# Kernel tuning notes

Hardware: AMD Instinct MI355X
Metric: run time of the kernel (lower is better)

Reference implementation:

```python
import jax, jax.numpy as jnp
import numpy as np

WIN = 7
SHIFT = 3
HEADS = 4
DIM = 128


def _rel_pos_index(wh, ww):
    coords = np.stack(np.meshgrid(np.arange(wh), np.arange(ww), indexing='ij')).reshape(2, -1)
    rel = (coords[:, :, None] - coords[:, None, :]).transpose(1, 2, 0)  # (N,N,2)
    rel[..., 0] += wh - 1
    rel[..., 1] += ww - 1
    rel[..., 0] *= 2 * ww - 1
    return rel.sum(-1)  # (N,N) int


def _shift_mask(H, W, wh, ww, sh, sw):
    img = np.zeros((H, W), dtype=np.float32)
    cnt = 0
    for hs in (slice(0, -wh), slice(-wh, -sh), slice(-sh, None)):
        for ws in (slice(0, -ww), slice(-ww, -sw), slice(-sw, None)):
            img[hs, ws] = cnt
            cnt += 1
    mw = img.reshape(H // wh, wh, W // ww, ww).transpose(0, 2, 1, 3).reshape(-1, wh * ww)
    diff = mw[:, :, None] - mw[:, None, :]
    return np.where(diff != 0, -100.0, 0.0).astype(np.float32)  # (nW,N,N)


def setup_inputs() -> dict:
    key = jax.random.key(0)
    ks = jax.random.split(key, 5)
    x = jax.random.normal(ks[0], (16, 112, 112, DIM), dtype=jnp.float32)
    w_qkv = jax.random.normal(ks[1], (DIM, 3 * DIM), dtype=jnp.float32) * 0.02
    b_qkv = jnp.zeros((3 * DIM,), dtype=jnp.float32)
    w_proj = jax.random.normal(ks[2], (DIM, DIM), dtype=jnp.float32) * 0.02
    b_proj = jnp.zeros((DIM,), dtype=jnp.float32)
    log_sigma = jnp.zeros((HEADS,), dtype=jnp.float32)  # sigma=1.0
    bias_table = jax.random.normal(ks[3], ((2 * WIN - 1) ** 2, HEADS), dtype=jnp.float32) * 0.02
    return {"x": x, "w_qkv": w_qkv, "b_qkv": b_qkv, "w_proj": w_proj,
            "b_proj": b_proj, "log_sigma": log_sigma, "bias_table": bias_table}


def reference(x, w_qkv, b_qkv, w_proj, b_proj, log_sigma, bias_table):
    B, H, W, C = x.shape
    wh = ww = WIN
    sh = sw = SHIFT
    heads = HEADS
    hd = C // heads
    N = wh * ww
    nWh, nWw = H // wh, W // ww

    shifted = jnp.roll(x, (-sh, -sw), axis=(1, 2))
    qkv = shifted @ w_qkv + b_qkv  # (B,H,W,3C)
    # window partition: -> (B*nW, 3, heads, N, hd)
    qkv = qkv.reshape(B, nWh, wh, nWw, ww, 3, heads, hd)
    qkv = qkv.transpose(0, 1, 3, 5, 6, 2, 4, 7).reshape(B * nWh * nWw, 3, heads, N, hd)
    q, k, v = qkv[:, 0], qkv[:, 1], qkv[:, 2]

    scale = hd ** -0.5
    q = q * scale
    k = k * scale
    q_sq = jnp.sum(q * q, -1, keepdims=True)               # (B_,h,N,1)
    k_sq = jnp.sum(k * k, -1, keepdims=True).swapaxes(-2, -1)  # (B_,h,1,N)
    qk = jnp.einsum('bhnd,bhmd->bhnm', q, k)
    dist_sq = jnp.maximum(q_sq + k_sq - 2.0 * qk, 1e-12)
    sigma_sq = jnp.exp(2.0 * log_sigma).reshape(1, heads, 1, 1)
    attn = (-0.5 / sigma_sq) * dist_sq                     # (B_,h,N,N)

    rpi = jnp.asarray(_rel_pos_index(wh, ww))
    bias = bias_table[rpi.reshape(-1)].reshape(N, N, heads).transpose(2, 0, 1)
    attn = attn + bias[None]

    mask = jnp.asarray(_shift_mask(H, W, wh, ww, sh, sw))  # (nW,N,N)
    attn = attn.reshape(B, nWh * nWw, heads, N, N) + mask[None, :, None]
    attn = jax.nn.softmax(attn, axis=-1).reshape(-1, heads, N, N)

    out = jnp.einsum('bhnm,bhmd->bhnd', attn, v)           # (B_,h,N,hd)
    out = out.transpose(0, 2, 1, 3).reshape(B, nWh, nWw, wh, ww, C)
    out = out.transpose(0, 1, 3, 2, 4, 5).reshape(B, H, W, C)
    out = jnp.roll(out, (sh, sw), axis=(1, 2))
    return out @ w_proj + b_proj
```

## Files before the change

kernel.cpp:

```cpp
#include <hip/hip_runtime.h>
#include <math.h>

#define IMG 112
#define CDIM 128
#define NTOK 49

__global__ __launch_bounds__(256, 4) void qkv_gemm_kernel(
    const float* __restrict__ x, const float* __restrict__ w,
    const float* __restrict__ bqkv, float* __restrict__ qkv)
{
    __shared__ float At[32][132];
    __shared__ float Bs[32][132];
    const int tid = threadIdx.x;
    const int m0 = blockIdx.x << 7;
    const int j0 = blockIdx.y << 7;
    const int tm = tid >> 4, tn = tid & 15;
    const float fscale = (j0 < 256) ? 0.17677669529663687f : 1.0f;

    float acc[8][8];
#pragma unroll
    for (int i = 0; i < 8; i++)
#pragma unroll
        for (int j = 0; j < 8; j++) acc[i][j] = 0.0f;

    for (int kc = 0; kc < 4; kc++) {
        if (kc) __syncthreads();
#pragma unroll
        for (int i = 0; i < 4; i++) {
            int idx = tid + (i << 8);
            int r = idx >> 3;
            int c4 = (idx & 7) << 2;
            int m = m0 + r;
            int b = m / (IMG * IMG);
            int rem = m - b * (IMG * IMG);
            int hh = rem / IMG;
            int ww_ = rem - hh * IMG;
            int hs = hh + 3; if (hs >= IMG) hs -= IMG;
            int ws = ww_ + 3; if (ws >= IMG) ws -= IMG;
            float4 v = *(const float4*)(x + ((size_t)((b * IMG + hs) * IMG + ws)) * CDIM + (kc << 5) + c4);
            At[c4 + 0][r] = v.x;
            At[c4 + 1][r] = v.y;
            At[c4 + 2][r] = v.z;
            At[c4 + 3][r] = v.w;
        }
#pragma unroll
        for (int i = 0; i < 4; i++) {
            int idx = tid + (i << 8);
            int c = idx >> 5;
            int j4 = (idx & 31) << 2;
            *(float4*)(&Bs[c][j4]) = *(const float4*)(w + (size_t)((kc << 5) + c) * 384 + j0 + j4);
        }
        __syncthreads();
#pragma unroll
        for (int c = 0; c < 32; c++) {
            float4 a0 = *(const float4*)(&At[c][tm << 2]);
            float4 a1 = *(const float4*)(&At[c][64 + (tm << 2)]);
            float4 b0 = *(const float4*)(&Bs[c][tn << 2]);
            float4 b1 = *(const float4*)(&Bs[c][64 + (tn << 2)]);
            float av[8] = {a0.x, a0.y, a0.z, a0.w, a1.x, a1.y, a1.z, a1.w};
            float bv[8] = {b0.x, b0.y, b0.z, b0.w, b1.x, b1.y, b1.z, b1.w};
#pragma unroll
            for (int ii = 0; ii < 8; ii++)
#pragma unroll
                for (int jj = 0; jj < 8; jj++) acc[ii][jj] = fmaf(av[ii], bv[jj], acc[ii][jj]);
        }
    }
    const int jb0 = j0 + (tn << 2);
    float4 bq0 = *(const float4*)(bqkv + jb0);
    float4 bq1 = *(const float4*)(bqkv + jb0 + 64);
#pragma unroll
    for (int ih = 0; ih < 2; ih++) {
#pragma unroll
        for (int ii = 0; ii < 4; ii++) {
            int r = (ih << 6) + (tm << 2) + ii;
            int m = m0 + r;
            int b = m / (IMG * IMG);
            int rem = m - b * (IMG * IMG);
            int hh = rem / IMG;
            int ww_ = rem - hh * IMG;
            int wi = hh / 7, ph = hh - wi * 7;
            int wj = ww_ / 7, pw = ww_ - wj * 7;
            size_t mp = (size_t)(((b * 16 + wi) * 16 + wj) * 49 + ph * 7 + pw);
            int ai = (ih << 2) + ii;
            float4 o0, o1;
            o0.x = (acc[ai][0] + bq0.x) * fscale;
            o0.y = (acc[ai][1] + bq0.y) * fscale;
            o0.z = (acc[ai][2] + bq0.z) * fscale;
            o0.w = (acc[ai][3] + bq0.w) * fscale;
            o1.x = (acc[ai][4] + bq1.x) * fscale;
            o1.y = (acc[ai][5] + bq1.y) * fscale;
            o1.z = (acc[ai][6] + bq1.z) * fscale;
            o1.w = (acc[ai][7] + bq1.w) * fscale;
            *(float4*)(qkv + mp * 384 + jb0) = o0;
            *(float4*)(qkv + mp * 384 + jb0 + 64) = o1;
        }
    }
}

#define KVSLAB 3136
#define OFF_BT 12544
#define SM_FLOATS 13220

__global__ __launch_bounds__(256, 3) void attn_kernel(
    const float* __restrict__ qkv, const float* __restrict__ wproj,
    const float* __restrict__ bproj, const float* __restrict__ lsig,
    const float* __restrict__ btab, float* __restrict__ out)
{
    __shared__ float sm[SM_FLOATS];
    const int tid = threadIdx.x;
    const int lane = tid & 63;
    const int h = tid >> 6;
    const int bx = blockIdx.x;
    const int wi = (bx >> 4) & 15;
    const int wj = bx & 15;

    float* kh  = sm + h * KVSLAB;
    float* vh  = kh + 1568;
    float* bts = sm + OFF_BT;
    float* osb = sm;
    float* wp  = sm + 6272;

    for (int i = tid; i < 676; i += 256) bts[i] = btab[i];

    const bool fi = (wi == 15), fj = (wj == 15);
    float4 q[8];
    float qsq = 0.0f, ks = 0.0f;
    int pbit = 0, qbit = 0, rbase = 0;

    const float* blkbase = qkv + (size_t)bx * (49 * 384);

    if (lane < NTOK) {
        int nh_ = lane / 7, nw_ = lane - (lane / 7) * 7;
        rbase = (nh_ * 13 + nw_) * 4 + h;
        pbit = (nh_ < 4) ? 1 : 0;
        qbit = (nw_ < 4) ? 1 : 0;
        const float* rowp = blkbase + lane * 384 + h * 32;
#pragma unroll
        for (int d4 = 0; d4 < 8; d4++) {
            float4 qv = *(const float4*)(rowp + (d4 << 2));
            q[d4] = qv;
            qsq = fmaf(qv.x, qv.x, qsq); qsq = fmaf(qv.y, qv.y, qsq);
            qsq = fmaf(qv.z, qv.z, qsq); qsq = fmaf(qv.w, qv.w, qsq);
            float4 kv = *(const float4*)(rowp + 128 + (d4 << 2));
            ks = fmaf(kv.x, kv.x, ks); ks = fmaf(kv.y, kv.y, ks);
            ks = fmaf(kv.z, kv.z, ks); ks = fmaf(kv.w, kv.w, ks);
            *(float4*)(kh + lane * 32 + ((d4 ^ (lane & 7)) << 2)) = kv;
            float4 vv = *(const float4*)(rowp + 256 + (d4 << 2));
            *(float4*)(vh + lane * 32 + ((d4 ^ (lane & 7)) << 2)) = vv;
        }
    }
    __syncthreads();

    float4 o[8];
#pragma unroll
    for (int d4 = 0; d4 < 8; d4++) { o[d4].x = 0.f; o[d4].y = 0.f; o[d4].z = 0.f; o[d4].w = 0.f; }
    float inv = 0.0f;

    if (lane < NTOK) {
        const float coef = -0.5f * __expf(-2.0f * lsig[h]);
        float s[49];
#pragma unroll
        for (int m = 0; m < 49; m++) {
            const int mh = m / 7, mw = m - (m / 7) * 7;
            float qk = 0.0f;
#pragma unroll
            for (int d4 = 0; d4 < 8; d4++) {
                float4 k4 = *(const float4*)(kh + m * 32 + ((d4 ^ (m & 7)) << 2));
                qk = fmaf(q[d4].x, k4.x, qk); qk = fmaf(q[d4].y, k4.y, qk);
                qk = fmaf(q[d4].z, k4.z, qk); qk = fmaf(q[d4].w, k4.w, qk);
            }
            float ksm = __shfl(ks, m, 64);
            float dist = fmaxf(qsq + ksm - 2.0f * qk, 1e-12f);
            float bias = bts[rbase + ((6 - mh) * 13 + (6 - mw)) * 4];
            int msk = (fi ? (pbit ^ ((mh < 4) ? 1 : 0)) : 0) | (fj ? (qbit ^ ((mw < 4) ? 1 : 0)) : 0);
            s[m] = fmaf(coef, dist, msk ? bias - 100.0f : bias);
        }
        float mx = s[0];
#pragma unroll
        for (int m = 1; m < 49; m++) mx = fmaxf(mx, s[m]);
        float sum = 0.0f;
#pragma unroll
        for (int m = 0; m < 49; m++) { float e = __expf(s[m] - mx); s[m] = e; sum += e; }
        inv = 1.0f / sum;
#pragma unroll
        for (int m = 0; m < 49; m++) {
            const float p = s[m];
#pragma unroll
            for (int d4 = 0; d4 < 8; d4++) {
                float4 v4 = *(const float4*)(vh + m * 32 + ((d4 ^ (m & 7)) << 2));
                o[d4].x = fmaf(p, v4.x, o[d4].x);
                o[d4].y = fmaf(p, v4.y, o[d4].y);
                o[d4].z = fmaf(p, v4.z, o[d4].z);
                o[d4].w = fmaf(p, v4.w, o[d4].w);
            }
        }
    }
    __syncthreads();

    if (lane < NTOK) {
#pragma unroll
        for (int d4 = 0; d4 < 8; d4++) {
            float4 ov;
            ov.x = o[d4].x * inv; ov.y = o[d4].y * inv;
            ov.z = o[d4].z * inv; ov.w = o[d4].w * inv;
            int gg = (h << 3) + d4;
            *(float4*)(osb + lane * 128 + ((gg ^ (lane & 7)) << 2)) = ov;
        }
    }
    for (int i = tid; i < 1024; i += 256)
        ((float4*)wp)[i] = ((const float4*)wproj)[i];
    __syncthreads();

    const int e4 = tid & 31;
    const int rowbase = tid >> 5;
    float4 bv = *(const float4*)(bproj + (e4 << 2));
    float4 pacc[7];
#pragma unroll
    for (int r = 0; r < 7; r++) pacc[r] = bv;

    for (int ch = 0; ch < 4; ch++) {
#pragma unroll 4
        for (int c4 = 0; c4 < 8; c4++) {
            const int cb = c4 << 2;
            float4 w0 = *(const float4*)(wp + (cb + 0) * 128 + (e4 << 2));
            float4 w1 = *(const float4*)(wp + (cb + 1) * 128 + (e4 << 2));
            float4 w2 = *(const float4*)(wp + (cb + 2) * 128 + (e4 << 2));
            float4 w3 = *(const float4*)(wp + (cb + 3) * 128 + (e4 << 2));
            const int gg = (ch << 3) + c4;
#pragma unroll
            for (int r = 0; r < 7; r++) {
                int nn = rowbase + (r << 3);
                if (nn < NTOK) {
                    float4 o4 = *(const float4*)(osb + nn * 128 + ((gg ^ (nn & 7)) << 2));
                    float4 a = pacc[r];
                    a.x = fmaf(o4.x, w0.x, a.x); a.y = fmaf(o4.x, w0.y, a.y);
                    a.z = fmaf(o4.x, w0.z, a.z); a.w = fmaf(o4.x, w0.w, a.w);
                    a.x = fmaf(o4.y, w1.x, a.x); a.y = fmaf(o4.y, w1.y, a.y);
                    a.z = fmaf(o4.y, w1.z, a.z); a.w = fmaf(o4.y, w1.w, a.w);
                    a.x = fmaf(o4.z, w2.x, a.x); a.y = fmaf(o4.z, w2.y, a.y);
                    a.z = fmaf(o4.z, w2.z, a.z); a.w = fmaf(o4.z, w2.w, a.w);
                    a.x = fmaf(o4.w, w3.x, a.x); a.y = fmaf(o4.w, w3.y, a.y);
                    a.z = fmaf(o4.w, w3.z, a.z); a.w = fmaf(o4.w, w3.w, a.w);
                    pacc[r] = a;
                }
            }
        }
        if (ch < 3) {
            __syncthreads();
            for (int i = tid; i < 1024; i += 256)
                ((float4*)wp)[i] = ((const float4*)(wproj + ((ch + 1) << 12)))[i];
            __syncthreads();
        }
    }
    const int b = bx >> 8;
#pragma unroll
    for (int r = 0; r < 7; r++) {
        int nn = rowbase + (r << 3);
        if (nn < NTOK) {
            int ph = nn / 7, pw = nn - (nn / 7) * 7;
            int ho = wi * 7 + ph + 3; if (ho >= IMG) ho -= IMG;
            int wo = wj * 7 + pw + 3; if (wo >= IMG) wo -= IMG;
            *(float4*)(out + ((size_t)((b * IMG + ho) * IMG + wo)) * CDIM + (e4 << 2)) = pacc[r];
        }
    }
}

extern "C" void kernel_launch(void* const* d_in, const int* in_sizes, int n_in,
                              void* d_out, int out_size, void* d_ws, size_t ws_size,
                              hipStream_t stream)
{
    const float* x         = (const float*)d_in[0];
    const float* w_qkv     = (const float*)d_in[1];
    const float* b_qkv     = (const float*)d_in[2];
    const float* w_proj    = (const float*)d_in[3];
    const float* b_proj    = (const float*)d_in[4];
    const float* log_sigma = (const float*)d_in[5];
    const float* bias_tab  = (const float*)d_in[6];
    float* out = (float*)d_out;
    float* qkv = (float*)d_ws;

    dim3 g1(200704 / 128, 3);
    qkv_gemm_kernel<<<g1, 256, 0, stream>>>(x, w_qkv, b_qkv, qkv);
    attn_kernel<<<4096, 256, 0, stream>>>(qkv, w_proj, b_proj, log_sigma, bias_tab, out);
}
```

Before: 708.6 us.

## Reorder QKV layout per head, prefetch GEMM tiles, read proj weights from global

The QKV GEMM now uses a 1D grid grouped so the three column chunks of the same row tiles run close together. It precomputes per-thread source pointers and register-prefetches the next K slice while computing the current one. The QKV intermediate is stored as [window][q/k/v][head][token][32], which makes each head's loads contiguous in the attention kernel. The projection stage drops its staged shared-memory copies of w_proj and reads weights straight from global/L2, removing three barrier pairs but adding redundant global loads per block.

```diff
diff --git a/kernel.cpp b/kernel.cpp
--- a/kernel.cpp
+++ b/kernel.cpp
@@ -12,45 +12,66 @@
     __shared__ float At[32][132];
     __shared__ float Bs[32][132];
     const int tid = threadIdx.x;
-    const int m0 = blockIdx.x << 7;
-    const int j0 = blockIdx.y << 7;
+    const int bid = blockIdx.x;
+    const int grp = bid / 24;
+    const int sub = bid - grp * 24;
+    const int jc  = sub >> 3;
+    const int m0  = (grp * 8 + (sub & 7)) << 7;
+    const int j0  = jc << 7;
     const int tm = tid >> 4, tn = tid & 15;
-    const float fscale = (j0 < 256) ? 0.17677669529663687f : 1.0f;
+    const float fscale = (jc < 2) ? 0.17677669529663687f : 1.0f;
+
+    const int c4A = (tid & 7) << 2;
+    const float* aptr[4];
+    int arow[4];
+#pragma unroll
+    for (int i = 0; i < 4; i++) {
+        int r = (tid >> 3) + (i << 5);
+        arow[i] = r;
+        int m = m0 + r;
+        int b = m / (IMG * IMG);
+        int rem = m - b * (IMG * IMG);
+        int hh = rem / IMG;
+        int ww_ = rem - hh * IMG;
+        int hs = hh + 3; if (hs >= IMG) hs -= IMG;
+        int ws = ww_ + 3; if (ws >= IMG) ws -= IMG;
+        aptr[i] = x + ((size_t)((b * IMG + hs) * IMG + ws)) * CDIM + c4A;
+    }
+    const int j4B = (tid & 31) << 2;
+    const int c0B = tid >> 5;
+    const float* bptr = w + (size_t)c0B * 384 + j0 + j4B;
 
     float acc[8][8];
 #pragma unroll
     for (int i = 0; i < 8; i++)
 #pragma unroll
         for (int j = 0; j < 8; j++) acc[i][j] = 0.0f;
+
+    float4 aR[4], bR[4];
+#pragma unroll
+    for (int i = 0; i < 4; i++) {
+        aR[i] = *(const float4*)(aptr[i]);
+        bR[i] = *(const float4*)(bptr + (size_t)(i << 3) * 384);
+    }
 
     for (int kc = 0; kc < 4; kc++) {
         if (kc) __syncthreads();
 #pragma unroll
         for (int i = 0; i < 4; i++) {
-            int idx = tid + (i << 8);
-            int r = idx >> 3;
-            int c4 = (idx & 7) << 2;
-            int m = m0 + r;
-            int b = m / (IMG * IMG);
-            int rem = m - b * (IMG * IMG);
-            int hh = rem / IMG;
-            int ww_ = rem - hh * IMG;
-            int hs = hh + 3; if (hs >= IMG) hs -= IMG;
-            int ws = ww_ + 3; if (ws >= IMG) ws -= IMG;
-            float4 v = *(const float4*)(x + ((size_t)((b * IMG + hs) * IMG + ws)) * CDIM + (kc << 5) + c4);
-            At[c4 + 0][r] = v.x;
-            At[c4 + 1][r] = v.y;
-            At[c4 + 2][r] = v.z;
-            At[c4 + 3][r] = v.w;
-        }
-#pragma unroll
-        for (int i = 0; i < 4; i++) {
-            int idx = tid + (i << 8);
-            int c = idx >> 5;
-            int j4 = (idx & 31) << 2;
-            *(float4*)(&Bs[c][j4]) = *(const float4*)(w + (size_t)((kc << 5) + c) * 384 + j0 + j4);
+            At[c4A + 0][arow[i]] = aR[i].x;
+            At[c4A + 1][arow[i]] = aR[i].y;
+            At[c4A + 2][arow[i]] = aR[i].z;
+            At[c4A + 3][arow[i]] = aR[i].w;
+            *(float4*)(&Bs[c0B + (i << 3)][j4B]) = bR[i];
         }
         __syncthreads();
+        if (kc < 3) {
+#pragma unroll
+            for (int i = 0; i < 4; i++) {
+                aR[i] = *(const float4*)(aptr[i] + ((kc + 1) << 5));
+                bR[i] = *(const float4*)(bptr + (size_t)((kc + 1) << 5) * 384 + (size_t)(i << 3) * 384);
+            }
+        }
 #pragma unroll
         for (int c = 0; c < 32; c++) {
             float4 a0 = *(const float4*)(&At[c][tm << 2]);
@@ -65,9 +86,11 @@
                 for (int jj = 0; jj < 8; jj++) acc[ii][jj] = fmaf(av[ii], bv[jj], acc[ii][jj]);
         }
     }
-    const int jb0 = j0 + (tn << 2);
-    float4 bq0 = *(const float4*)(bqkv + jb0);
-    float4 bq1 = *(const float4*)(bqkv + jb0 + 64);
+
+    const int hA = tn >> 3;
+    const int dd = (tn & 7) << 2;
+    float4 bq0 = *(const float4*)(bqkv + j0 + (tn << 2));
+    float4 bq1 = *(const float4*)(bqkv + j0 + 64 + (tn << 2));
 #pragma unroll
     for (int ih = 0; ih < 2; ih++) {
 #pragma unroll
@@ -80,7 +103,8 @@
             int ww_ = rem - hh * IMG;
             int wi = hh / 7, ph = hh - wi * 7;
             int wj = ww_ / 7, pw = ww_ - wj * 7;
-            size_t mp = (size_t)(((b * 16 + wi) * 16 + wj) * 49 + ph * 7 + pw);
+            size_t basew = (size_t)(((b * 16 + wi) * 16 + wj)) * 18816
+                         + (size_t)jc * 6272 + (size_t)(ph * 7 + pw) * 32 + dd;
             int ai = (ih << 2) + ii;
             float4 o0, o1;
             o0.x = (acc[ai][0] + bq0.x) * fscale;
@@ -91,8 +115,8 @@
             o1.y = (acc[ai][5] + bq1.y) * fscale;
             o1.z = (acc[ai][6] + bq1.z) * fscale;
             o1.w = (acc[ai][7] + bq1.w) * fscale;
-            *(float4*)(qkv + mp * 384 + jb0) = o0;
-            *(float4*)(qkv + mp * 384 + jb0 + 64) = o1;
+            *(float4*)(qkv + basew + (size_t)hA * 1568) = o0;
+            *(float4*)(qkv + basew + (size_t)(2 + hA) * 1568) = o1;
         }
     }
 }
@@ -118,7 +142,6 @@
     float* vh  = kh + 1568;
     float* bts = sm + OFF_BT;
     float* osb = sm;
-    float* wp  = sm + 6272;
 
     for (int i = tid; i < 676; i += 256) bts[i] = btab[i];
 
@@ -127,25 +150,24 @@
     float qsq = 0.0f, ks = 0.0f;
     int pbit = 0, qbit = 0, rbase = 0;
 
-    const float* blkbase = qkv + (size_t)bx * (49 * 384);
+    const float* basep = qkv + (size_t)bx * 18816 + (size_t)h * 1568 + lane * 32;
 
     if (lane < NTOK) {
         int nh_ = lane / 7, nw_ = lane - (lane / 7) * 7;
         rbase = (nh_ * 13 + nw_) * 4 + h;
         pbit = (nh_ < 4) ? 1 : 0;
         qbit = (nw_ < 4) ? 1 : 0;
-        const float* rowp = blkbase + lane * 384 + h * 32;
 #pragma unroll
         for (int d4 = 0; d4 < 8; d4++) {
-            float4 qv = *(const float4*)(rowp + (d4 << 2));
+            float4 qv = *(const float4*)(basep + (d4 << 2));
             q[d4] = qv;
             qsq = fmaf(qv.x, qv.x, qsq); qsq = fmaf(qv.y, qv.y, qsq);
             qsq = fmaf(qv.z, qv.z, qsq); qsq = fmaf(qv.w, qv.w, qsq);
-            float4 kv = *(const float4*)(rowp + 128 + (d4 << 2));
+            float4 kv = *(const float4*)(basep + 6272 + (d4 << 2));
             ks = fmaf(kv.x, kv.x, ks); ks = fmaf(kv.y, kv.y, ks);
             ks = fmaf(kv.z, kv.z, ks); ks = fmaf(kv.w, kv.w, ks);
             *(float4*)(kh + lane * 32 + ((d4 ^ (lane & 7)) << 2)) = kv;
-            float4 vv = *(const float4*)(rowp + 256 + (d4 << 2));
+            float4 vv = *(const float4*)(basep + 12544 + (d4 << 2));
             *(float4*)(vh + lane * 32 + ((d4 ^ (lane & 7)) << 2)) = vv;
         }
     }
@@ -207,8 +229,6 @@
             *(float4*)(osb + lane * 128 + ((gg ^ (lane & 7)) << 2)) = ov;
         }
     }
-    for (int i = tid; i < 1024; i += 256)
-        ((float4*)wp)[i] = ((const float4*)wproj)[i];
     __syncthreads();
 
     const int e4 = tid & 31;
@@ -218,38 +238,29 @@
 #pragma unroll
     for (int r = 0; r < 7; r++) pacc[r] = bv;
 
-    for (int ch = 0; ch < 4; ch++) {
 #pragma unroll 4
-        for (int c4 = 0; c4 < 8; c4++) {
-            const int cb = c4 << 2;
-            float4 w0 = *(const float4*)(wp + (cb + 0) * 128 + (e4 << 2));
-            float4 w1 = *(const float4*)(wp + (cb + 1) * 128 + (e4 << 2));
-            float4 w2 = *(const float4*)(wp + (cb + 2) * 128 + (e4 << 2));
-            float4 w3 = *(const float4*)(wp + (cb + 3) * 128 + (e4 << 2));
-            const int gg = (ch << 3) + c4;
-#pragma unroll
-            for (int r = 0; r < 7; r++) {
-                int nn = rowbase + (r << 3);
-                if (nn < NTOK) {
-                    float4 o4 = *(const float4*)(osb + nn * 128 + ((gg ^ (nn & 7)) << 2));
-                    float4 a = pacc[r];
-                    a.x = fmaf(o4.x, w0.x, a.x); a.y = fmaf(o4.x, w0.y, a.y);
-                    a.z = fmaf(o4.x, w0.z, a.z); a.w = fmaf(o4.x, w0.w, a.w);
-                    a.x = fmaf(o4.y, w1.x, a.x); a.y = fmaf(o4.y, w1.y, a.y);
-                    a.z = fmaf(o4.y, w1.z, a.z); a.w = fmaf(o4.y, w1.w, a.w);
-                    a.x = fmaf(o4.z, w2.x, a.x); a.y = fmaf(o4.z, w2.y, a.y);
-                    a.z = fmaf(o4.z, w2.z, a.z); a.w = fmaf(o4.z, w2.w, a.w);
-                    a.x = fmaf(o4.w, w3.x, a.x); a.y = fmaf(o4.w, w3.y, a.y);
-                    a.z = fmaf(o4.w, w3.z, a.z); a.w = fmaf(o4.w, w3.w, a.w);
-                    pacc[r] = a;
-                }
-            }
-        }
-        if (ch < 3) {
-            __syncthreads();
-            for (int i = tid; i < 1024; i += 256)
-                ((float4*)wp)[i] = ((const float4*)(wproj + ((ch + 1) << 12)))[i];
-            __syncthreads();
+    for (int c = 0; c < 32; c++) {
+        const float* wr = wproj + ((c << 2) * 128) + (e4 << 2);
+        float4 w0 = *(const float4*)(wr);
+        float4 w1 = *(const float4*)(wr + 128);
+        float4 w2 = *(const float4*)(wr + 256);
+        float4 w3 = *(const float4*)(wr + 384);
+#pragma unroll
+        for (int r = 0; r < 7; r++) {
+            int nn = rowbase + (r << 3);
+            if (nn < NTOK) {
+                float4 o4 = *(const float4*)(osb + nn * 128 + ((c ^ (nn & 7)) << 2));
+                float4 a = pacc[r];
+                a.x = fmaf(o4.x, w0.x, a.x); a.y = fmaf(o4.x, w0.y, a.y);
+                a.z = fmaf(o4.x, w0.z, a.z); a.w = fmaf(o4.x, w0.w, a.w);
+                a.x = fmaf(o4.y, w1.x, a.x); a.y = fmaf(o4.y, w1.y, a.y);
+                a.z = fmaf(o4.y, w1.z, a.z); a.w = fmaf(o4.y, w1.w, a.w);
+                a.x = fmaf(o4.z, w2.x, a.x); a.y = fmaf(o4.z, w2.y, a.y);
+                a.z = fmaf(o4.z, w2.z, a.z); a.w = fmaf(o4.z, w2.w, a.w);
+                a.x = fmaf(o4.w, w3.x, a.x); a.y = fmaf(o4.w, w3.y, a.y);
+                a.z = fmaf(o4.w, w3.z, a.z); a.w = fmaf(o4.w, w3.w, a.w);
+                pacc[r] = a;
+            }
         }
     }
     const int b = bx >> 8;
@@ -279,7 +290,6 @@
     float* out = (float*)d_out;
     float* qkv = (float*)d_ws;
 
-    dim3 g1(200704 / 128, 3);
-    qkv_gemm_kernel<<<g1, 256, 0, stream>>>(x, w_qkv, b_qkv, qkv);
+    qkv_gemm_kernel<<<4704, 256, 0, stream>>>(x, w_qkv, b_qkv, qkv);
     attn_kernel<<<4096, 256, 0, stream>>>(qkv, w_proj, b_proj, log_sigma, bias_tab, out);
 }
```

After: 1.172 ms. +65.4%, slower.
